# Kernel optimization log

Measured on AMD Instinct MI355X. Metric: run time of the kernel, lower is better.

The kernel has to match this reference:

```python
import jax, jax.numpy as jnp
import numpy as np

B, N, C = 2048, 49, 768
MID = 48  # 768 // 16
SELECT_SIZES = (36, 24)  # int(49*0.75), int(49*0.5)
LN_EPS = 1e-5


def _hier_se(x, w1, b1, w2, b2):
    """HierarchicalSE: SE gating + importance scores. x: [B, N, C]."""
    s = x.mean(axis=1)  # [B, C]
    h = jax.nn.gelu(s @ w1 + b1, approximate=False)
    gates = jax.nn.sigmoid(h @ w2 + b2)[:, None, :]  # [B, 1, C]
    out = x * gates
    ts = jnp.linalg.norm(out, axis=-1)  # [B, N]
    ts = ts - ts.mean(axis=-1, keepdims=True)
    std = jnp.std(ts, axis=-1, ddof=1, keepdims=True) + 1e-6  # torch std is unbiased
    importance = jax.nn.softmax(ts / std, axis=-1)
    return out, importance


def _select_patches(tokens, importance, k):
    _, idx = jax.lax.top_k(importance, k)  # [B, k]
    return jnp.take_along_axis(tokens, idx[:, :, None], axis=1)  # [B, k, C]


def setup_inputs() -> dict:
    key = jax.random.key(0)
    ks = jax.random.split(key, 8)
    sc = 0.02
    return {
        "x": jax.random.normal(ks[0], (B, N, C), dtype=jnp.float32),
        "se1_w1": jax.random.normal(ks[1], (C, MID), dtype=jnp.float32) * sc,
        "se1_b1": jnp.zeros((MID,), jnp.float32),
        "se1_w2": jax.random.normal(ks[2], (MID, C), dtype=jnp.float32) * sc,
        "se1_b2": jnp.zeros((C,), jnp.float32),
        "se2_w1": jax.random.normal(ks[3], (C, MID), dtype=jnp.float32) * sc,
        "se2_b1": jnp.zeros((MID,), jnp.float32),
        "se2_w2": jax.random.normal(ks[4], (MID, C), dtype=jnp.float32) * sc,
        "se2_b2": jnp.zeros((C,), jnp.float32),
        "ln_gamma": jnp.ones((C,), jnp.float32),
        "ln_beta": jnp.zeros((C,), jnp.float32),
        "cls_w": jax.random.normal(ks[5], (C, 5), dtype=jnp.float32) * sc,
        "cls_b": jnp.zeros((5,), jnp.float32),
    }


def reference(x, se1_w1, se1_b1, se1_w2, se1_b2,
              se2_w1, se2_b1, se2_w2, se2_b2,
              ln_gamma, ln_beta, cls_w, cls_b):
    tokens = x
    params = ((se1_w1, se1_b1, se1_w2, se1_b2), (se2_w1, se2_b1, se2_w2, se2_b2))
    for (w1, b1, w2, b2), k in zip(params, SELECT_SIZES):
        tokens_attn, importance = _hier_se(tokens, w1, b1, w2, b2)
        tokens = _select_patches(tokens_attn, importance, k)
    pooled = tokens.mean(axis=1)  # [B, C]
    mu = pooled.mean(axis=-1, keepdims=True)
    var = pooled.var(axis=-1, keepdims=True)
    normed = (pooled - mu) * jax.lax.rsqrt(var + LN_EPS) * ln_gamma + ln_beta
    return normed @ cls_w + cls_b  # [B, 5]
```

## Files before the change

### kernel.cpp

```cpp
#include <hip/hip_runtime.h>
#include <math.h>

#define NB    2048
#define NTOK  49
#define CH    768
#define MID   48
#define K1    36
#define K2    24
#define NTHR  512
#define NWAVE (NTHR/64)

__device__ __forceinline__ float wsum(float v) {
    #pragma unroll
    for (int off = 32; off; off >>= 1) v += __shfl_xor(v, off, 64);
    return v;
}

__global__ __launch_bounds__(NTHR, 2)
void hier_se_fused(const float* __restrict__ x,
                   const float* __restrict__ w1a, const float* __restrict__ b1a,
                   const float* __restrict__ w2a, const float* __restrict__ b2a,
                   const float* __restrict__ w1b, const float* __restrict__ b1b,
                   const float* __restrict__ w2b, const float* __restrict__ b2b,
                   const float* __restrict__ lng, const float* __restrict__ lnb,
                   const float* __restrict__ cw,  const float* __restrict__ cb,
                   float* __restrict__ out)
{
    __shared__ __align__(16) float tok[NTOK*CH];
    __shared__ float sA[CH];
    __shared__ float g1[CH];
    __shared__ float g12[CH];
    __shared__ float hb[MID];
    __shared__ float red[NWAVE*MID];
    __shared__ float ts[64];
    __shared__ int   sel1[K1];
    __shared__ int   sel2[K2];
    __shared__ float scal[2];

    const int tid  = threadIdx.x;
    const int lane = tid & 63;
    const int wv   = tid >> 6;
    const int b    = blockIdx.x;

    {
        const float4* src = (const float4*)(x + (size_t)b * (NTOK*CH));
        float4* dst = (float4*)tok;
        #pragma unroll
        for (int k = 0; k < 19; ++k) {
            int i = k*NTHR + tid;
            if (i < NTOK*CH/4) dst[i] = src[i];
        }
    }
    float wreg[96];
    {
        const int ml = lane < MID ? lane : MID-1;
        const float* wp = w1a + (96*wv)*MID + ml;
        #pragma unroll
        for (int k = 0; k < 96; ++k) wreg[k] = wp[k*MID];
    }
    __syncthreads();

    for (int c = tid; c < CH; c += NTHR) {
        float a0 = tok[48*CH + c], a1 = 0.f;
        #pragma unroll
        for (int n = 0; n < 48; n += 2) { a0 += tok[n*CH+c]; a1 += tok[(n+1)*CH+c]; }
        sA[c] = (a0 + a1) * (1.0f/NTOK);
    }
    __syncthreads();

    {
        float a0=0.f,a1=0.f,a2=0.f,a3=0.f;
        #pragma unroll
        for (int k = 0; k < 96; k += 4) {
            a0 = fmaf(wreg[k+0], sA[96*wv+k+0], a0);
            a1 = fmaf(wreg[k+1], sA[96*wv+k+1], a1);
            a2 = fmaf(wreg[k+2], sA[96*wv+k+2], a2);
            a3 = fmaf(wreg[k+3], sA[96*wv+k+3], a3);
        }
        if (lane < MID) red[wv*MID + lane] = (a0+a1)+(a2+a3);
    }
    {
        const int ml = lane < MID ? lane : MID-1;
        const float* wp = w1b + (96*wv)*MID + ml;
        #pragma unroll
        for (int k = 0; k < 96; ++k) wreg[k] = wp[k*MID];
    }
    __syncthreads();
    if (tid < MID) {
        float v = b1a[tid];
        #pragma unroll
        for (int w = 0; w < NWAVE; ++w) v += red[w*MID + tid];
        hb[tid] = 0.5f * v * (1.0f + erff(v * 0.70710678118654752440f));
    }
    __syncthreads();

    for (int c = tid; c < CH; c += NTHR) {
        float a0=0.f,a1=0.f,a2=0.f,a3=0.f;
        #pragma unroll
        for (int m = 0; m < MID; m += 4) {
            a0 = fmaf(hb[m+0], w2a[(m+0)*CH + c], a0);
            a1 = fmaf(hb[m+1], w2a[(m+1)*CH + c], a1);
            a2 = fmaf(hb[m+2], w2a[(m+2)*CH + c], a2);
            a3 = fmaf(hb[m+3], w2a[(m+3)*CH + c], a3);
        }
        float v = b2a[c] + ((a0+a1)+(a2+a3));
        g1[c] = 1.0f / (1.0f + expf(-v));
    }
    __syncthreads();

    for (int n = wv; n < NTOK; n += NWAVE) {
        float acc = 0.f;
        #pragma unroll
        for (int k = 0; k < CH/64; ++k) {
            int c = lane + k*64;
            float v = tok[n*CH + c] * g1[c];
            acc = fmaf(v, v, acc);
        }
        acc = wsum(acc);
        if (lane == 0) ts[n] = sqrtf(acc);
    }
    __syncthreads();

    if (wv == 0) {
        float vl = (lane < NTOK) ? ts[lane] : -1.0f;
        int rank = 0;
        for (int j = 0; j < NTOK; ++j) {
            float vj = ts[j];
            rank += (vj > vl) || (vj == vl && j < lane);
        }
        if (lane < NTOK && rank < K1) sel1[rank] = lane;
    }
    __syncthreads();

    {
        int rows[K1];
        #pragma unroll
        for (int r = 0; r < K1; ++r) rows[r] = sel1[r]*CH;
        for (int c = tid; c < CH; c += NTHR) {
            float a0=0.f,a1=0.f;
            #pragma unroll
            for (int r = 0; r < K1; r += 2) { a0 += tok[rows[r]+c]; a1 += tok[rows[r+1]+c]; }
            sA[c] = (a0+a1) * (1.0f/K1) * g1[c];
        }
    }
    __syncthreads();

    {
        float a0=0.f,a1=0.f,a2=0.f,a3=0.f;
        #pragma unroll
        for (int k = 0; k < 96; k += 4) {
            a0 = fmaf(wreg[k+0], sA[96*wv+k+0], a0);
            a1 = fmaf(wreg[k+1], sA[96*wv+k+1], a1);
            a2 = fmaf(wreg[k+2], sA[96*wv+k+2], a2);
            a3 = fmaf(wreg[k+3], sA[96*wv+k+3], a3);
        }
        if (lane < MID) red[wv*MID + lane] = (a0+a1)+(a2+a3);
    }
    __syncthreads();
    if (tid < MID) {
        float v = b1b[tid];
        #pragma unroll
        for (int w = 0; w < NWAVE; ++w) v += red[w*MID + tid];
        hb[tid] = 0.5f * v * (1.0f + erff(v * 0.70710678118654752440f));
    }
    __syncthreads();

    for (int c = tid; c < CH; c += NTHR) {
        float a0=0.f,a1=0.f,a2=0.f,a3=0.f;
        #pragma unroll
        for (int m = 0; m < MID; m += 4) {
            a0 = fmaf(hb[m+0], w2b[(m+0)*CH + c], a0);
            a1 = fmaf(hb[m+1], w2b[(m+1)*CH + c], a1);
            a2 = fmaf(hb[m+2], w2b[(m+2)*CH + c], a2);
            a3 = fmaf(hb[m+3], w2b[(m+3)*CH + c], a3);
        }
        float v = b2b[c] + ((a0+a1)+(a2+a3));
        g12[c] = g1[c] * (1.0f / (1.0f + expf(-v)));
    }
    __syncthreads();

    for (int j = wv; j < K1; j += NWAVE) {
        int base = sel1[j]*CH;
        float acc = 0.f;
        #pragma unroll
        for (int k = 0; k < CH/64; ++k) {
            int c = lane + k*64;
            float v = tok[base + c] * g12[c];
            acc = fmaf(v, v, acc);
        }
        acc = wsum(acc);
        if (lane == 0) ts[j] = sqrtf(acc);
    }
    __syncthreads();

    if (wv == 0) {
        float vl = (lane < K1) ? ts[lane] : -1.0f;
        int rank = 0;
        for (int j = 0; j < K1; ++j) {
            float vj = ts[j];
            rank += (vj > vl) || (vj == vl && j < lane);
        }
        if (lane < K1 && rank < K2) sel2[rank] = sel1[lane];
    }
    __syncthreads();

    {
        int rows[K2];
        #pragma unroll
        for (int r = 0; r < K2; ++r) rows[r] = sel2[r]*CH;
        for (int c = tid; c < CH; c += NTHR) {
            float a0=0.f,a1=0.f;
            #pragma unroll
            for (int r = 0; r < K2; r += 2) { a0 += tok[rows[r]+c]; a1 += tok[rows[r+1]+c]; }
            sA[c] = (a0+a1) * (1.0f/K2) * g12[c];
        }
    }
    __syncthreads();

    if (wv == 0) {
        float s = 0.f, q = 0.f;
        #pragma unroll
        for (int k = 0; k < CH/64; ++k) {
            float v = sA[lane + k*64];
            s += v; q = fmaf(v, v, q);
        }
        s = wsum(s); q = wsum(q);
        if (lane == 0) {
            float mu  = s * (1.0f/CH);
            float var = q * (1.0f/CH) - mu*mu;
            scal[0] = mu;
            scal[1] = rsqrtf(var + 1e-5f);
        }
    }
    __syncthreads();

    if (wv < 5) {
        const float mu = scal[0], inv = scal[1];
        float acc = 0.f;
        #pragma unroll
        for (int k = 0; k < CH/64; ++k) {
            int c = lane + k*64;
            float nv = (sA[c] - mu) * inv * lng[c] + lnb[c];
            acc = fmaf(nv, cw[c*5 + wv], acc);
        }
        acc = wsum(acc);
        if (lane == 0) out[b*5 + wv] = acc + cb[wv];
    }
}

extern "C" void kernel_launch(void* const* d_in, const int* in_sizes, int n_in,
                              void* d_out, int out_size, void* d_ws, size_t ws_size,
                              hipStream_t stream) {
    (void)in_sizes; (void)n_in; (void)d_ws; (void)ws_size; (void)out_size;
    const float* x   = (const float*)d_in[0];
    const float* w1a = (const float*)d_in[1];
    const float* b1a = (const float*)d_in[2];
    const float* w2a = (const float*)d_in[3];
    const float* b2a = (const float*)d_in[4];
    const float* w1b = (const float*)d_in[5];
    const float* b1b = (const float*)d_in[6];
    const float* w2b = (const float*)d_in[7];
    const float* b2b = (const float*)d_in[8];
    const float* lng = (const float*)d_in[9];
    const float* lnb = (const float*)d_in[10];
    const float* cw  = (const float*)d_in[11];
    const float* cb  = (const float*)d_in[12];
    float* out = (float*)d_out;

    hipLaunchKernelGGL(hier_se_fused, dim3(NB), dim3(NTHR), 0, stream,
                       x, w1a, b1a, w2a, b2a, w1b, b1b, w2b, b2b,
                       lng, lnb, cw, cb, out);
}
```

Before: 601.1 us.

## Split fused per-sample kernel into multi-kernel pipeline with batched SE GEMVs

Replaces the single per-batch fused kernel, which held all 49 tokens in LDS, with seven kernels. They compute column sums, batched SE GEMVs that reuse weights across 8 or 32 samples, norm/top-k selection, and a final selection/pool/LayerNorm/classifier, passing intermediates through workspace. This targets the low occupancy from the ~150KB-per-block LDS footprint and the per-sample re-reading of the SE weights. In exchange, x is read from global memory about three times instead of once, and there is extra launch and workspace traffic. The fused kernel is kept as a fallback when the workspace is too small.

```diff
diff --git a/kernel.cpp b/kernel.cpp
--- a/kernel.cpp
+++ b/kernel.cpp
@@ -7,15 +7,258 @@
 #define MID   48
 #define K1    36
 #define K2    24
-#define NTHR  512
-#define NWAVE (NTHR/64)
 
 __device__ __forceinline__ float wsum(float v) {
     #pragma unroll
     for (int off = 32; off; off >>= 1) v += __shfl_xor(v, off, 64);
     return v;
 }
-
+__device__ __forceinline__ float gelu_exact(float v) {
+    return 0.5f * v * (1.0f + erff(v * 0.70710678118654752440f));
+}
+__device__ __forceinline__ float sigmoidf(float v) {
+    return 1.0f / (1.0f + expf(-v));
+}
+
+__global__ __launch_bounds__(384)
+void ka_colsum(const float* __restrict__ x, float* __restrict__ colsum)
+{
+    __shared__ float4 part[2][192];
+    const int tid = threadIdx.x;
+    const int c4 = tid % 192;
+    const int n0 = tid / 192;
+    const int b  = blockIdx.x;
+    const float4* xb = (const float4*)(x + (size_t)b * (NTOK*CH));
+    float4 acc = {0.f,0.f,0.f,0.f};
+    for (int n = n0; n < NTOK; n += 2) {
+        float4 v = xb[n*192 + c4];
+        acc.x += v.x; acc.y += v.y; acc.z += v.z; acc.w += v.w;
+    }
+    part[n0][c4] = acc;
+    __syncthreads();
+    if (tid < 192) {
+        float4 a = part[0][tid], q = part[1][tid];
+        float4 r; r.x=a.x+q.x; r.y=a.y+q.y; r.z=a.z+q.z; r.w=a.w+q.w;
+        ((float4*)colsum)[(size_t)b*192 + tid] = r;
+    }
+}
+
+__global__ __launch_bounds__(384)
+void kb_gemv1(const float* __restrict__ sin, const float* __restrict__ w1,
+              const float* __restrict__ b1, float* __restrict__ h, float scale)
+{
+    __shared__ float lds_s[8][772];
+    const int tid = threadIdx.x;
+    const int base = blockIdx.x * 8;
+    #pragma unroll
+    for (int k = 0; k < 4; ++k) {
+        int i = tid + 384*k;
+        int bb = i / 192, c4 = i % 192;
+        float4 v = ((const float4*)sin)[(size_t)(base+bb)*192 + c4];
+        *(float4*)&lds_s[bb][4*c4] = v;
+    }
+    __syncthreads();
+    const int m  = tid % MID;
+    const int bg = tid / MID;
+    float acc = 0.f;
+    #pragma unroll 8
+    for (int c = 0; c < CH; ++c)
+        acc = fmaf(lds_s[bg][c], w1[c*MID + m], acc);
+    h[(size_t)(base+bg)*MID + m] = gelu_exact(acc * scale + b1[m]);
+}
+
+__global__ __launch_bounds__(256)
+void kc_gemv2(const float* __restrict__ h, const float* __restrict__ w2,
+              const float* __restrict__ b2, const float* __restrict__ gmul,
+              float* __restrict__ gout)
+{
+    __shared__ float lh[32][MID];
+    const int tid  = threadIdx.x;
+    const int base = blockIdx.x * 32;
+    const int c    = blockIdx.y * 256 + tid;
+    #pragma unroll
+    for (int k = 0; k < 6; ++k) {
+        int i = tid + 256*k;
+        int bb = i / MID, m = i % MID;
+        lh[bb][m] = h[(size_t)(base+bb)*MID + m];
+    }
+    __syncthreads();
+    float wr[MID];
+    #pragma unroll
+    for (int m = 0; m < MID; ++m) wr[m] = w2[(size_t)m*CH + c];
+    const float bias = b2[c];
+    for (int bb = 0; bb < 32; ++bb) {
+        float acc = bias;
+        #pragma unroll
+        for (int m = 0; m < MID; ++m) acc = fmaf(lh[bb][m], wr[m], acc);
+        float g = sigmoidf(acc);
+        size_t o = (size_t)(base+bb)*CH + c;
+        gout[o] = gmul ? gmul[o] * g : g;
+    }
+}
+
+__global__ __launch_bounds__(512)
+void kd_norm_select(const float* __restrict__ x, const float* __restrict__ g1,
+                    float* __restrict__ s2, int* __restrict__ sel1g)
+{
+    __shared__ float g1v[CH];
+    __shared__ float gsq[CH];
+    __shared__ float ts[64];
+    __shared__ int   seln[K1];
+    const int tid = threadIdx.x, lane = tid & 63, wv = tid >> 6;
+    const int b = NB - 1 - blockIdx.x;
+    const float* xb = x + (size_t)b * (NTOK*CH);
+
+    for (int c = tid; c < CH; c += 512) {
+        float g = g1[(size_t)b*CH + c];
+        g1v[c] = g; gsq[c] = g*g;
+    }
+    __syncthreads();
+
+    float gs[12];
+    #pragma unroll
+    for (int k = 0; k < 3; ++k) {
+        float4 q = *(const float4*)&gsq[4*lane + 256*k];
+        gs[4*k+0]=q.x; gs[4*k+1]=q.y; gs[4*k+2]=q.z; gs[4*k+3]=q.w;
+    }
+
+    for (int n = wv; n < NTOK; n += 8) {
+        const float4* row = (const float4*)(xb + n*CH);
+        float acc = 0.f;
+        #pragma unroll
+        for (int k = 0; k < 3; ++k) {
+            float4 v = row[lane + 64*k];
+            acc = fmaf(v.x*v.x, gs[4*k+0], acc);
+            acc = fmaf(v.y*v.y, gs[4*k+1], acc);
+            acc = fmaf(v.z*v.z, gs[4*k+2], acc);
+            acc = fmaf(v.w*v.w, gs[4*k+3], acc);
+        }
+        acc = wsum(acc);
+        if (lane == 0) ts[n] = sqrtf(acc);
+    }
+    __syncthreads();
+
+    if (wv == 0) {
+        float vl = (lane < NTOK) ? ts[lane] : -1.0f;
+        int rank = 0;
+        for (int j = 0; j < NTOK; ++j) {
+            float vj = ts[j];
+            rank += (vj > vl) || (vj == vl && j < lane);
+        }
+        if (lane < NTOK && rank < K1) { seln[rank] = lane; sel1g[(size_t)b*K1 + rank] = lane; }
+    }
+    __syncthreads();
+
+    int rows[K1];
+    #pragma unroll
+    for (int r = 0; r < K1; ++r) rows[r] = seln[r]*CH;
+    for (int c = tid; c < CH; c += 512) {
+        float a0=0.f, a1=0.f;
+        #pragma unroll
+        for (int r = 0; r < K1; r += 2) { a0 += xb[rows[r]+c]; a1 += xb[rows[r+1]+c]; }
+        s2[(size_t)b*CH + c] = (a0+a1) * (1.0f/K1) * g1v[c];
+    }
+}
+
+__global__ __launch_bounds__(512)
+void kg_final(const float* __restrict__ x, const float* __restrict__ g12,
+              const int* __restrict__ sel1g,
+              const float* __restrict__ lng, const float* __restrict__ lnb,
+              const float* __restrict__ cw,  const float* __restrict__ cb,
+              float* __restrict__ out)
+{
+    __shared__ float g12v[CH];
+    __shared__ float pooled[CH];
+    __shared__ float ts2[K1];
+    __shared__ int   nrow[K1];
+    __shared__ int   selrows[K2];
+    __shared__ float scal[2];
+    const int tid = threadIdx.x, lane = tid & 63, wv = tid >> 6;
+    const int b = blockIdx.x;
+    const float* xb = x + (size_t)b * (NTOK*CH);
+
+    for (int c = tid; c < CH; c += 512) g12v[c] = g12[(size_t)b*CH + c];
+    if (tid < K1) nrow[tid] = sel1g[(size_t)b*K1 + tid];
+    __syncthreads();
+
+    float gr[12];
+    #pragma unroll
+    for (int k = 0; k < 3; ++k) {
+        float4 q = *(const float4*)&g12v[4*lane + 256*k];
+        gr[4*k+0]=q.x; gr[4*k+1]=q.y; gr[4*k+2]=q.z; gr[4*k+3]=q.w;
+    }
+
+    for (int j = wv; j < K1; j += 8) {
+        const float4* row = (const float4*)(xb + nrow[j]*CH);
+        float acc = 0.f;
+        #pragma unroll
+        for (int k = 0; k < 3; ++k) {
+            float4 v = row[lane + 64*k];
+            acc = fmaf(v.x*v.x, gr[4*k+0]*gr[4*k+0], acc);
+            acc = fmaf(v.y*v.y, gr[4*k+1]*gr[4*k+1], acc);
+            acc = fmaf(v.z*v.z, gr[4*k+2]*gr[4*k+2], acc);
+            acc = fmaf(v.w*v.w, gr[4*k+3]*gr[4*k+3], acc);
+        }
+        acc = wsum(acc);
+        if (lane == 0) ts2[j] = sqrtf(acc);
+    }
+    __syncthreads();
+
+    if (wv == 0) {
+        float vl = (lane < K1) ? ts2[lane] : -1.0f;
+        int rank = 0;
+        for (int j = 0; j < K1; ++j) {
+            float vj = ts2[j];
+            rank += (vj > vl) || (vj == vl && j < lane);
+        }
+        if (lane < K1 && rank < K2) selrows[rank] = nrow[lane];
+    }
+    __syncthreads();
+
+    int rows[K2];
+    #pragma unroll
+    for (int r = 0; r < K2; ++r) rows[r] = selrows[r]*CH;
+    for (int c = tid; c < CH; c += 512) {
+        float a0=0.f, a1=0.f;
+        #pragma unroll
+        for (int r = 0; r < K2; r += 2) { a0 += xb[rows[r]+c]; a1 += xb[rows[r+1]+c]; }
+        pooled[c] = (a0+a1) * (1.0f/K2) * g12v[c];
+    }
+    __syncthreads();
+
+    if (wv == 0) {
+        float s = 0.f, q = 0.f;
+        #pragma unroll
+        for (int k = 0; k < CH/64; ++k) {
+            float v = pooled[lane + 64*k];
+            s += v; q = fmaf(v, v, q);
+        }
+        s = wsum(s); q = wsum(q);
+        if (lane == 0) {
+            float mu  = s * (1.0f/CH);
+            float var = q * (1.0f/CH) - mu*mu;
+            scal[0] = mu;
+            scal[1] = rsqrtf(var + 1e-5f);
+        }
+    }
+    __syncthreads();
+
+    if (wv < 5) {
+        const float mu = scal[0], inv = scal[1];
+        float acc = 0.f;
+        #pragma unroll
+        for (int k = 0; k < CH/64; ++k) {
+            int c = lane + 64*k;
+            float nv = (pooled[c] - mu) * inv * lng[c] + lnb[c];
+            acc = fmaf(nv, cw[c*5 + wv], acc);
+        }
+        acc = wsum(acc);
+        if (lane == 0) out[(size_t)b*5 + wv] = acc + cb[wv];
+    }
+}
+
+#define NTHR 512
+#define NWAVE (NTHR/64)
 __global__ __launch_bounds__(NTHR, 2)
 void hier_se_fused(const float* __restrict__ x,
                    const float* __restrict__ w1a, const float* __restrict__ b1a,
@@ -90,7 +333,7 @@
         float v = b1a[tid];
         #pragma unroll
         for (int w = 0; w < NWAVE; ++w) v += red[w*MID + tid];
-        hb[tid] = 0.5f * v * (1.0f + erff(v * 0.70710678118654752440f));
+        hb[tid] = gelu_exact(v);
     }
     __syncthreads();
 
@@ -103,8 +346,7 @@
             a2 = fmaf(hb[m+2], w2a[(m+2)*CH + c], a2);
             a3 = fmaf(hb[m+3], w2a[(m+3)*CH + c], a3);
         }
-        float v = b2a[c] + ((a0+a1)+(a2+a3));
-        g1[c] = 1.0f / (1.0f + expf(-v));
+        g1[c] = sigmoidf(b2a[c] + ((a0+a1)+(a2+a3)));
     }
     __syncthreads();
 
@@ -161,7 +403,7 @@
         float v = b1b[tid];
         #pragma unroll
         for (int w = 0; w < NWAVE; ++w) v += red[w*MID + tid];
-        hb[tid] = 0.5f * v * (1.0f + erff(v * 0.70710678118654752440f));
+        hb[tid] = gelu_exact(v);
     }
     __syncthreads();
 
@@ -174,8 +416,7 @@
             a2 = fmaf(hb[m+2], w2b[(m+2)*CH + c], a2);
             a3 = fmaf(hb[m+3], w2b[(m+3)*CH + c], a3);
         }
-        float v = b2b[c] + ((a0+a1)+(a2+a3));
-        g12[c] = g1[c] * (1.0f / (1.0f + expf(-v)));
+        g12[c] = g1[c] * sigmoidf(b2b[c] + ((a0+a1)+(a2+a3)));
     }
     __syncthreads();
 
@@ -251,7 +492,7 @@
 extern "C" void kernel_launch(void* const* d_in, const int* in_sizes, int n_in,
                               void* d_out, int out_size, void* d_ws, size_t ws_size,
                               hipStream_t stream) {
-    (void)in_sizes; (void)n_in; (void)d_ws; (void)ws_size; (void)out_size;
+    (void)in_sizes; (void)n_in; (void)out_size;
     const float* x   = (const float*)d_in[0];
     const float* w1a = (const float*)d_in[1];
     const float* b1a = (const float*)d_in[2];
@@ -267,7 +508,30 @@
     const float* cb  = (const float*)d_in[12];
     float* out = (float*)d_out;
 
-    hipLaunchKernelGGL(hier_se_fused, dim3(NB), dim3(NTHR), 0, stream,
-                       x, w1a, b1a, w2a, b2a, w1b, b1b, w2b, b2b,
-                       lng, lnb, cw, cb, out);
-}
+    const size_t need = ((size_t)2*NB*CH + (size_t)NB*MID) * 4 + (size_t)NB*K1*4;
+    if (ws_size < need) {
+        hipLaunchKernelGGL(hier_se_fused, dim3(NB), dim3(NTHR), 0, stream,
+                           x, w1a, b1a, w2a, b2a, w1b, b1b, w2b, b2b,
+                           lng, lnb, cw, cb, out);
+        return;
+    }
+
+    float* buf0 = (float*)d_ws;
+    float* buf1 = buf0 + (size_t)NB*CH;
+    float* hbuf = buf1 + (size_t)NB*CH;
+    int*   sel1 = (int*)(hbuf + (size_t)NB*MID);
+
+    hipLaunchKernelGGL(ka_colsum, dim3(NB), dim3(384), 0, stream, x, buf0);
+    hipLaunchKernelGGL(kb_gemv1, dim3(NB/8), dim3(384), 0, stream,
+                       buf0, w1a, b1a, hbuf, 1.0f/NTOK);
+    hipLaunchKernelGGL(kc_gemv2, dim3(NB/32, 3), dim3(256), 0, stream,
+                       hbuf, w2a, b2a, (const float*)nullptr, buf1);
+    hipLaunchKernelGGL(kd_norm_select, dim3(NB), dim3(512), 0, stream,
+                       x, buf1, buf0, sel1);
+    hipLaunchKernelGGL(kb_gemv1, dim3(NB/8), dim3(384), 0, stream,
+                       buf0, w1b, b1b, hbuf, 1.0f);
+    hipLaunchKernelGGL(kc_gemv2, dim3(NB/32, 3), dim3(256), 0, stream,
+                       hbuf, w2b, b2b, buf1, buf1);
+    hipLaunchKernelGGL(kg_final, dim3(NB), dim3(512), 0, stream,
+                       x, buf1, sel1, lng, lnb, cw, cb, out);
+}
```

Measured after the change: 687.5 us. 1.14x slower.

## Drop shared-memory token tile; stream rows from global with subtraction-based pooled means

Applied to the files above, without the earlier changes.

Removes the ~150KB per-block shared-memory copy of the token matrix, so several blocks can share a CU (launch bounds go from 2 to 6 blocks of 384 threads). Token norms and pooled means are read directly from global/L2 instead of LDS. Selected-token means come from subtracting the unselected rows from the full column sum, which touches far fewer rows. The squared gates are precomputed per lane. The cost is repeated global reads of x rows, which now rely on cache hits, and a slightly different floating-point summation order.

```diff
diff --git a/kernel.cpp b/kernel.cpp
--- a/kernel.cpp
+++ b/kernel.cpp
@@ -7,117 +7,118 @@
 #define MID   48
 #define K1    36
 #define K2    24
-#define NTHR  512
-#define NWAVE (NTHR/64)
+#define NU1   (NTOK - K1)
+#define NU2   (K1 - K2)
+#define NTHR  384
 
 __device__ __forceinline__ float wsum(float v) {
     #pragma unroll
     for (int off = 32; off; off >>= 1) v += __shfl_xor(v, off, 64);
     return v;
 }
-
-__global__ __launch_bounds__(NTHR, 2)
-void hier_se_fused(const float* __restrict__ x,
-                   const float* __restrict__ w1a, const float* __restrict__ b1a,
-                   const float* __restrict__ w2a, const float* __restrict__ b2a,
-                   const float* __restrict__ w1b, const float* __restrict__ b1b,
-                   const float* __restrict__ w2b, const float* __restrict__ b2b,
-                   const float* __restrict__ lng, const float* __restrict__ lnb,
-                   const float* __restrict__ cw,  const float* __restrict__ cb,
-                   float* __restrict__ out)
+__device__ __forceinline__ float gelu_exact(float v) {
+    return 0.5f * v * (1.0f + erff(v * 0.70710678118654752440f));
+}
+__device__ __forceinline__ float sigmoidf(float v) {
+    return 1.0f / (1.0f + expf(-v));
+}
+
+__global__ __launch_bounds__(NTHR, 6)
+void fused_all(const float* __restrict__ x,
+               const float* __restrict__ w1a, const float* __restrict__ b1a,
+               const float* __restrict__ w2a, const float* __restrict__ b2a,
+               const float* __restrict__ w1b, const float* __restrict__ b1b,
+               const float* __restrict__ w2b, const float* __restrict__ b2b,
+               const float* __restrict__ lng, const float* __restrict__ lnb,
+               const float* __restrict__ cw,  const float* __restrict__ cb,
+               float* __restrict__ out)
 {
-    __shared__ __align__(16) float tok[NTOK*CH];
+    __shared__ float colsum[CH];
     __shared__ float sA[CH];
-    __shared__ float g1[CH];
-    __shared__ float g12[CH];
+    __shared__ float gv[CH];
+    __shared__ float red[8 * MID];
     __shared__ float hb[MID];
-    __shared__ float red[NWAVE*MID];
     __shared__ float ts[64];
     __shared__ int   sel1[K1];
-    __shared__ int   sel2[K2];
+    __shared__ int   unsel1[NU1];
+    __shared__ int   unsel2[NU2];
     __shared__ float scal[2];
 
     const int tid  = threadIdx.x;
     const int lane = tid & 63;
     const int wv   = tid >> 6;
     const int b    = blockIdx.x;
-
-    {
-        const float4* src = (const float4*)(x + (size_t)b * (NTOK*CH));
-        float4* dst = (float4*)tok;
-        #pragma unroll
-        for (int k = 0; k < 19; ++k) {
-            int i = k*NTHR + tid;
-            if (i < NTOK*CH/4) dst[i] = src[i];
-        }
-    }
-    float wreg[96];
-    {
-        const int ml = lane < MID ? lane : MID-1;
-        const float* wp = w1a + (96*wv)*MID + ml;
-        #pragma unroll
-        for (int k = 0; k < 96; ++k) wreg[k] = wp[k*MID];
-    }
-    __syncthreads();
-
-    for (int c = tid; c < CH; c += NTHR) {
-        float a0 = tok[48*CH + c], a1 = 0.f;
-        #pragma unroll
-        for (int n = 0; n < 48; n += 2) { a0 += tok[n*CH+c]; a1 += tok[(n+1)*CH+c]; }
-        sA[c] = (a0 + a1) * (1.0f/NTOK);
-    }
-    __syncthreads();
-
-    {
-        float a0=0.f,a1=0.f,a2=0.f,a3=0.f;
-        #pragma unroll
-        for (int k = 0; k < 96; k += 4) {
-            a0 = fmaf(wreg[k+0], sA[96*wv+k+0], a0);
-            a1 = fmaf(wreg[k+1], sA[96*wv+k+1], a1);
-            a2 = fmaf(wreg[k+2], sA[96*wv+k+2], a2);
-            a3 = fmaf(wreg[k+3], sA[96*wv+k+3], a3);
-        }
-        if (lane < MID) red[wv*MID + lane] = (a0+a1)+(a2+a3);
-    }
-    {
-        const int ml = lane < MID ? lane : MID-1;
-        const float* wp = w1b + (96*wv)*MID + ml;
-        #pragma unroll
-        for (int k = 0; k < 96; ++k) wreg[k] = wp[k*MID];
+    const float* xb = x + (size_t)b * (NTOK * CH);
+
+    {
+        const float2* p = (const float2*)xb;
+        float sx = 0.f, sy = 0.f;
+        #pragma unroll 7
+        for (int n = 0; n < NTOK; ++n) {
+            float2 v = p[n * 384 + tid];
+            sx += v.x; sy += v.y;
+        }
+        colsum[2*tid]   = sx;
+        colsum[2*tid+1] = sy;
+    }
+    __syncthreads();
+
+    {
+        const int m = tid % MID, ch = tid / MID;
+        const float* wp = w1a + (ch * 96) * MID + m;
+        const float* sp = colsum + ch * 96;
+        float a = 0.f;
+        #pragma unroll
+        for (int k = 0; k < 96; ++k) a = fmaf(sp[k], wp[k * MID], a);
+        red[ch * MID + m] = a;
     }
     __syncthreads();
     if (tid < MID) {
-        float v = b1a[tid];
-        #pragma unroll
-        for (int w = 0; w < NWAVE; ++w) v += red[w*MID + tid];
-        hb[tid] = 0.5f * v * (1.0f + erff(v * 0.70710678118654752440f));
-    }
-    __syncthreads();
-
-    for (int c = tid; c < CH; c += NTHR) {
-        float a0=0.f,a1=0.f,a2=0.f,a3=0.f;
-        #pragma unroll
-        for (int m = 0; m < MID; m += 4) {
-            a0 = fmaf(hb[m+0], w2a[(m+0)*CH + c], a0);
-            a1 = fmaf(hb[m+1], w2a[(m+1)*CH + c], a1);
-            a2 = fmaf(hb[m+2], w2a[(m+2)*CH + c], a2);
-            a3 = fmaf(hb[m+3], w2a[(m+3)*CH + c], a3);
-        }
-        float v = b2a[c] + ((a0+a1)+(a2+a3));
-        g1[c] = 1.0f / (1.0f + expf(-v));
-    }
-    __syncthreads();
-
-    for (int n = wv; n < NTOK; n += NWAVE) {
-        float acc = 0.f;
-        #pragma unroll
-        for (int k = 0; k < CH/64; ++k) {
-            int c = lane + k*64;
-            float v = tok[n*CH + c] * g1[c];
-            acc = fmaf(v, v, acc);
-        }
-        acc = wsum(acc);
-        if (lane == 0) ts[n] = sqrtf(acc);
+        float v = 0.f;
+        #pragma unroll
+        for (int c = 0; c < 8; ++c) v += red[c * MID + tid];
+        hb[tid] = gelu_exact(v * (1.0f / NTOK) + b1a[tid]);
+    }
+    __syncthreads();
+
+    {
+        const float2* w2r = (const float2*)w2a;
+        float2 bb = ((const float2*)b2a)[tid];
+        float a0 = bb.x, a1 = bb.y;
+        #pragma unroll
+        for (int m = 0; m < MID; ++m) {
+            float2 w = w2r[(size_t)m * 384 + tid];
+            float h = hb[m];
+            a0 = fmaf(h, w.x, a0);
+            a1 = fmaf(h, w.y, a1);
+        }
+        gv[2*tid]   = sigmoidf(a0);
+        gv[2*tid+1] = sigmoidf(a1);
+    }
+    __syncthreads();
+
+    {
+        float gs[12];
+        #pragma unroll
+        for (int k = 0; k < 3; ++k) {
+            float4 q = *(const float4*)&gv[4*lane + 256*k];
+            gs[4*k+0] = q.x*q.x; gs[4*k+1] = q.y*q.y;
+            gs[4*k+2] = q.z*q.z; gs[4*k+3] = q.w*q.w;
+        }
+        for (int n = wv; n < NTOK; n += 6) {
+            const float4* row = (const float4*)(xb + n * CH);
+            float acc = 0.f;
+            #pragma unroll
+            for (int k = 0; k < 3; ++k) {
+                float4 v = row[lane + 64*k];
+                acc = fmaf(v.x*v.x, gs[4*k+0], acc);
+                acc = fmaf(v.y*v.y, gs[4*k+1], acc);
+                acc = fmaf(v.z*v.z, gs[4*k+2], acc);
+                acc = fmaf(v.w*v.w, gs[4*k+3], acc);
+            }
+            acc = wsum(acc);
+            if (lane == 0) ts[n] = sqrtf(acc);
+        }
     }
     __syncthreads();
 
@@ -128,68 +129,86 @@
             float vj = ts[j];
             rank += (vj > vl) || (vj == vl && j < lane);
         }
-        if (lane < NTOK && rank < K1) sel1[rank] = lane;
-    }
-    __syncthreads();
-
-    {
-        int rows[K1];
-        #pragma unroll
-        for (int r = 0; r < K1; ++r) rows[r] = sel1[r]*CH;
-        for (int c = tid; c < CH; c += NTHR) {
-            float a0=0.f,a1=0.f;
+        if (lane < NTOK) {
+            if (rank < K1) sel1[rank] = lane;
+            else           unsel1[rank - K1] = lane;
+        }
+    }
+    __syncthreads();
+
+    {
+        int rows[NU1];
+        #pragma unroll
+        for (int r = 0; r < NU1; ++r) rows[r] = unsel1[r] * CH;
+        float2 cs = *(float2*)&colsum[2*tid];
+        #pragma unroll
+        for (int r = 0; r < NU1; ++r) {
+            float2 v = *(const float2*)(xb + rows[r] + 2*tid);
+            cs.x -= v.x; cs.y -= v.y;
+        }
+        *(float2*)&colsum[2*tid] = cs;
+        float2 g = *(float2*)&gv[2*tid];
+        sA[2*tid]   = cs.x * (1.0f / K1) * g.x;
+        sA[2*tid+1] = cs.y * (1.0f / K1) * g.y;
+    }
+    __syncthreads();
+
+    {
+        const int m = tid % MID, ch = tid / MID;
+        const float* wp = w1b + (ch * 96) * MID + m;
+        const float* sp = sA + ch * 96;
+        float a = 0.f;
+        #pragma unroll
+        for (int k = 0; k < 96; ++k) a = fmaf(sp[k], wp[k * MID], a);
+        red[ch * MID + m] = a;
+    }
+    __syncthreads();
+    if (tid < MID) {
+        float v = 0.f;
+        #pragma unroll
+        for (int c = 0; c < 8; ++c) v += red[c * MID + tid];
+        hb[tid] = gelu_exact(v + b1b[tid]);
+    }
+    __syncthreads();
+
+    {
+        const float2* w2r = (const float2*)w2b;
+        float2 bb = ((const float2*)b2b)[tid];
+        float a0 = bb.x, a1 = bb.y;
+        #pragma unroll
+        for (int m = 0; m < MID; ++m) {
+            float2 w = w2r[(size_t)m * 384 + tid];
+            float h = hb[m];
+            a0 = fmaf(h, w.x, a0);
+            a1 = fmaf(h, w.y, a1);
+        }
+        gv[2*tid]   *= sigmoidf(a0);
+        gv[2*tid+1] *= sigmoidf(a1);
+    }
+    __syncthreads();
+
+    {
+        float gr[12];
+        #pragma unroll
+        for (int k = 0; k < 3; ++k) {
+            float4 q = *(const float4*)&gv[4*lane + 256*k];
+            gr[4*k+0] = q.x*q.x; gr[4*k+1] = q.y*q.y;
+            gr[4*k+2] = q.z*q.z; gr[4*k+3] = q.w*q.w;
+        }
+        for (int j = wv; j < K1; j += 6) {
+            const float4* row = (const float4*)(xb + sel1[j] * CH);
+            float acc = 0.f;
             #pragma unroll
-            for (int r = 0; r < K1; r += 2) { a0 += tok[rows[r]+c]; a1 += tok[rows[r+1]+c]; }
-            sA[c] = (a0+a1) * (1.0f/K1) * g1[c];
-        }
-    }
-    __syncthreads();
-
-    {
-        float a0=0.f,a1=0.f,a2=0.f,a3=0.f;
-        #pragma unroll
-        for (int k = 0; k < 96; k += 4) {
-            a0 = fmaf(wreg[k+0], sA[96*wv+k+0], a0);
-            a1 = fmaf(wreg[k+1], sA[96*wv+k+1], a1);
-            a2 = fmaf(wreg[k+2], sA[96*wv+k+2], a2);
-            a3 = fmaf(wreg[k+3], sA[96*wv+k+3], a3);
-        }
-        if (lane < MID) red[wv*MID + lane] = (a0+a1)+(a2+a3);
-    }
-    __syncthreads();
-    if (tid < MID) {
-        float v = b1b[tid];
-        #pragma unroll
-        for (int w = 0; w < NWAVE; ++w) v += red[w*MID + tid];
-        hb[tid] = 0.5f * v * (1.0f + erff(v * 0.70710678118654752440f));
-    }
-    __syncthreads();
-
-    for (int c = tid; c < CH; c += NTHR) {
-        float a0=0.f,a1=0.f,a2=0.f,a3=0.f;
-        #pragma unroll
-        for (int m = 0; m < MID; m += 4) {
-            a0 = fmaf(hb[m+0], w2b[(m+0)*CH + c], a0);
-            a1 = fmaf(hb[m+1], w2b[(m+1)*CH + c], a1);
-            a2 = fmaf(hb[m+2], w2b[(m+2)*CH + c], a2);
-            a3 = fmaf(hb[m+3], w2b[(m+3)*CH + c], a3);
-        }
-        float v = b2b[c] + ((a0+a1)+(a2+a3));
-        g12[c] = g1[c] * (1.0f / (1.0f + expf(-v)));
-    }
-    __syncthreads();
-
-    for (int j = wv; j < K1; j += NWAVE) {
-        int base = sel1[j]*CH;
-        float acc = 0.f;
-        #pragma unroll
-        for (int k = 0; k < CH/64; ++k) {
-            int c = lane + k*64;
-            float v = tok[base + c] * g12[c];
-            acc = fmaf(v, v, acc);
-        }
-        acc = wsum(acc);
-        if (lane == 0) ts[j] = sqrtf(acc);
+            for (int k = 0; k < 3; ++k) {
+                float4 v = row[lane + 64*k];
+                acc = fmaf(v.x*v.x, gr[4*k+0], acc);
+                acc = fmaf(v.y*v.y, gr[4*k+1], acc);
+                acc = fmaf(v.z*v.z, gr[4*k+2], acc);
+                acc = fmaf(v.w*v.w, gr[4*k+3], acc);
+            }
+            acc = wsum(acc);
+            if (lane == 0) ts[j] = sqrtf(acc);
+        }
     }
     __syncthreads();
 
@@ -200,20 +219,23 @@
             float vj = ts[j];
             rank += (vj > vl) || (vj == vl && j < lane);
         }
-        if (lane < K1 && rank < K2) sel2[rank] = sel1[lane];
-    }
-    __syncthreads();
-
-    {
-        int rows[K2];
-        #pragma unroll
-        for (int r = 0; r < K2; ++r) rows[r] = sel2[r]*CH;
-        for (int c = tid; c < CH; c += NTHR) {
-            float a0=0.f,a1=0.f;
-            #pragma unroll
-            for (int r = 0; r < K2; r += 2) { a0 += tok[rows[r]+c]; a1 += tok[rows[r+1]+c]; }
-            sA[c] = (a0+a1) * (1.0f/K2) * g12[c];
-        }
+        if (lane < K1 && rank >= K2) unsel2[rank - K2] = sel1[lane];
+    }
+    __syncthreads();
+
+    {
+        int rows[NU2];
+        #pragma unroll
+        for (int r = 0; r < NU2; ++r) rows[r] = unsel2[r] * CH;
+        float2 cs = *(float2*)&colsum[2*tid];
+        #pragma unroll
+        for (int r = 0; r < NU2; ++r) {
+            float2 v = *(const float2*)(xb + rows[r] + 2*tid);
+            cs.x -= v.x; cs.y -= v.y;
+        }
+        float2 g = *(float2*)&gv[2*tid];
+        sA[2*tid]   = cs.x * (1.0f / K2) * g.x;
+        sA[2*tid+1] = cs.y * (1.0f / K2) * g.y;
     }
     __syncthreads();
 
@@ -221,13 +243,13 @@
         float s = 0.f, q = 0.f;
         #pragma unroll
         for (int k = 0; k < CH/64; ++k) {
-            float v = sA[lane + k*64];
+            float v = sA[lane + 64*k];
             s += v; q = fmaf(v, v, q);
         }
         s = wsum(s); q = wsum(q);
         if (lane == 0) {
-            float mu  = s * (1.0f/CH);
-            float var = q * (1.0f/CH) - mu*mu;
+            float mu  = s * (1.0f / CH);
+            float var = q * (1.0f / CH) - mu * mu;
             scal[0] = mu;
             scal[1] = rsqrtf(var + 1e-5f);
         }
@@ -239,19 +261,19 @@
         float acc = 0.f;
         #pragma unroll
         for (int k = 0; k < CH/64; ++k) {
-            int c = lane + k*64;
+            int c = lane + 64*k;
             float nv = (sA[c] - mu) * inv * lng[c] + lnb[c];
             acc = fmaf(nv, cw[c*5 + wv], acc);
         }
         acc = wsum(acc);
-        if (lane == 0) out[b*5 + wv] = acc + cb[wv];
+        if (lane == 0) out[(size_t)b*5 + wv] = acc + cb[wv];
     }
 }
 
 extern "C" void kernel_launch(void* const* d_in, const int* in_sizes, int n_in,
                               void* d_out, int out_size, void* d_ws, size_t ws_size,
                               hipStream_t stream) {
-    (void)in_sizes; (void)n_in; (void)d_ws; (void)ws_size; (void)out_size;
+    (void)in_sizes; (void)n_in; (void)out_size; (void)d_ws; (void)ws_size;
     const float* x   = (const float*)d_in[0];
     const float* w1a = (const float*)d_in[1];
     const float* b1a = (const float*)d_in[2];
@@ -267,7 +289,7 @@
     const float* cb  = (const float*)d_in[12];
     float* out = (float*)d_out;
 
-    hipLaunchKernelGGL(hier_se_fused, dim3(NB), dim3(NTHR), 0, stream,
+    hipLaunchKernelGGL(fused_all, dim3(NB), dim3(NTHR), 0, stream,
                        x, w1a, b1a, w2a, b2a, w1b, b1b, w2b, b2b,
                        lng, lnb, cw, cb, out);
 }
```

After: 546.0 us. 9.2% less time.
